# Optimization experiments

Hardware: AMD Instinct MI355X
Metric: run time of the kernel (lower is better)

Reference implementation:

```python
import jax, jax.numpy as jnp
import numpy as np

DIM = 128  # matches init kwarg `dim`; scale = dim ** 0.5


def setup_inputs() -> dict:
    key = jax.random.key(0)
    k1, k2, k3, k4 = jax.random.split(key, 4)
    A = 100000
    K = 1600000  # num edges
    z_msg_all = jax.random.normal(k1, (A, DIM), dtype=jnp.float32)
    recv_query_all = jax.random.normal(k2, (A, DIM), dtype=jnp.float32)
    i_idx = jax.random.randint(k3, (K,), 0, A, dtype=jnp.int64)
    j_idx = jax.random.randint(k4, (K,), 0, A, dtype=jnp.int64)
    return {"z_msg_all": z_msg_all, "recv_query_all": recv_query_all,
            "i_idx": i_idx, "j_idx": j_idx, "A": A}


def reference(z_msg_all, recv_query_all, i_idx, j_idx, A):
    # q_j = z[j], k_i = z[i]; per-edge scores; segmented softmax over recipient j;
    # weighted scatter-add of values k_i into pooled[j]. recv_query_all is unused
    # in the original forward (kept for signature fidelity).
    scale = DIM ** 0.5
    k = z_msg_all[i_idx]                     # (K, D) gather
    q = z_msg_all[j_idx]                     # (K, D) gather
    scores = jnp.sum(q * k, axis=-1) / scale  # (K,)
    # segmented softmax (3-pass: amax, exp, sum)
    max_per = jax.ops.segment_max(scores, j_idx, num_segments=A)  # (A,)
    exp = jnp.exp(scores - max_per[j_idx])                         # (K,)
    denom = jax.ops.segment_sum(exp, j_idx, num_segments=A)        # (A,)
    alpha = exp / (denom[j_idx] + 1e-6)                            # (K,)
    # weighted scatter-add of values into recipients
    pooled = jax.ops.segment_sum(alpha[:, None] * k, j_idx, num_segments=A)  # (A, D)
    return pooled
```

## Files before the change

### kernel.cpp

```cpp
#include <hip/hip_runtime.h>
#include <math.h>


typedef unsigned short us8 __attribute__((ext_vector_type(8)));
typedef float f32x2 __attribute__((ext_vector_type(2)));

#define CAP  8192
#define ABLK 512
#define EPB  (ABLK * 8)

__device__ inline unsigned short f2bf(float f) {
    unsigned u = __float_as_uint(f);
    return (unsigned short)((u + 0x7fff + ((u >> 16) & 1)) >> 16);
}
__device__ inline float bfhi(unsigned u) { return __uint_as_float(u & 0xffff0000u); }
__device__ inline float bflo(unsigned u) { return __uint_as_float(u << 16); }

__global__ __launch_bounds__(ABLK) void bin_kernel(
        const float* __restrict__ z, us8* __restrict__ z16,
        const int* __restrict__ i_idx, const int* __restrict__ j_idx,
        int* __restrict__ gcount, unsigned* __restrict__ binned,
        int n16, int K, int NB) {
    int tid = threadIdx.x;
    int t0 = blockIdx.x * ABLK + tid;
    int nth = gridDim.x * ABLK;

    const float4* __restrict__ z4 = reinterpret_cast<const float4*>(z);
    #pragma unroll
    for (int q = 0; q < 8; ++q) {
        int t = t0 + q * nth;
        if (t < n16) {
            float4 a = z4[(size_t)2 * t];
            float4 c = z4[(size_t)2 * t + 1];
            us8 o;
            o[0] = f2bf(a.x); o[1] = f2bf(a.y); o[2] = f2bf(a.z); o[3] = f2bf(a.w);
            o[4] = f2bf(c.x); o[5] = f2bf(c.y); o[6] = f2bf(c.z); o[7] = f2bf(c.w);
            z16[t] = o;
        }
    }

    __shared__ int lhist[ABLK];
    __shared__ int loff[ABLK + 1];
    __shared__ int lcur[ABLK];
    __shared__ int gbase[ABLK];
    __shared__ unsigned staged_p[EPB];
    __shared__ unsigned short staged_b[EPB];

    lhist[tid] = 0;
    __syncthreads();

    int ebase = blockIdx.x * EPB;
    int myi[8], myj[8], myb[8];
    #pragma unroll
    for (int q = 0; q < 8; ++q) {
        int e = ebase + tid + q * ABLK;
        if (e < K) {
            myj[q] = j_idx[e];
            myi[q] = i_idx[e];
            myb[q] = myj[q] >> 8;
            atomicAdd(&lhist[myb[q]], 1);
        } else {
            myb[q] = -1;
        }
    }
    __syncthreads();
    for (int off = 1; off < ABLK; off <<= 1) {
        int v = (tid >= off) ? lhist[tid - off] : 0;
        __syncthreads();
        lhist[tid] += v;
        __syncthreads();
    }
    loff[tid + 1] = lhist[tid];
    if (tid == 0) loff[0] = 0;
    __syncthreads();
    int cntb = loff[tid + 1] - loff[tid];
    if (tid < NB && cntb > 0)
        gbase[tid] = tid * CAP + atomicAdd(&gcount[tid], cntb);
    lcur[tid] = loff[tid];
    __syncthreads();
    #pragma unroll
    for (int q = 0; q < 8; ++q) {
        if (myb[q] >= 0) {
            int p = atomicAdd(&lcur[myb[q]], 1);
            staged_p[p] = ((unsigned)myi[q] << 8) | ((unsigned)myj[q] & 255u);
            staged_b[p] = (unsigned short)myb[q];
        }
    }
    __syncthreads();
    int totE = loff[ABLK];
    for (int idx = tid; idx < totE; idx += ABLK) {
        int bb = staged_b[idx];
        binned[(size_t)gbase[bb] + (idx - loff[bb])] = staged_p[idx];
    }
}

__global__ __launch_bounds__(1024) void finish_kernel(
        unsigned* __restrict__ binned, const int* __restrict__ gcount,
        int2* __restrict__ seg, int A) {
    __shared__ unsigned staged[CAP];
    __shared__ int sorted_loc[CAP];
    __shared__ int hist[256];
    __shared__ int offs[257];
    __shared__ int cur[256];

    int b = blockIdx.x;
    int tid = threadIdx.x;
    int cnt = gcount[b];
    if (cnt > CAP) cnt = CAP;
    unsigned* __restrict__ src = binned + (size_t)b * CAP;

    if (tid < 256) hist[tid] = 0;
    for (int x = tid; x < cnt; x += 1024) staged[x] = src[x];
    __syncthreads();
    for (int x = tid; x < cnt; x += 1024)
        atomicAdd(&hist[staged[x] & 255u], 1);
    __syncthreads();
    for (int off = 1; off < 256; off <<= 1) {
        int v = 0;
        if (tid < 256 && tid >= off) v = hist[tid - off];
        __syncthreads();
        if (tid < 256 && tid >= off) hist[tid] += v;
        __syncthreads();
    }
    if (tid == 0) offs[0] = 0;
    if (tid < 256) offs[tid + 1] = hist[tid];
    __syncthreads();
    if (tid < 256) cur[tid] = offs[tid];
    __syncthreads();
    for (int x = tid; x < cnt; x += 1024) {
        unsigned pk = staged[x];
        int p = atomicAdd(&cur[pk & 255u], 1);
        sorted_loc[p] = (int)(pk >> 8);
    }
    __syncthreads();
    for (int x = tid; x < cnt; x += 1024) src[x] = (unsigned)sorted_loc[x];
    if (tid < 256) {
        int j = (b << 8) + tid;
        if (j < A)
            seg[j] = make_int2(b * CAP + offs[tid], b * CAP + offs[tid + 1]);
    }
}

__global__ __launch_bounds__(256) void attn_kernel(
        const float* __restrict__ z, const us8* __restrict__ z16,
        const unsigned* __restrict__ sorted_i, const int2* __restrict__ seg,
        float* __restrict__ out, int A) {
    int w = blockIdx.x * 4 + (threadIdx.x >> 6);
    if (w >= A) return;
    int lane = threadIdx.x & 63;
    int g = lane >> 3;
    int r = lane & 7;

    const float4* __restrict__ z4 = reinterpret_cast<const float4*>(z);
    size_t qb = (size_t)w * 32;
    float4 a0 = z4[qb + 2 * r];
    float4 a1 = z4[qb + 2 * r + 1];
    float4 a2 = z4[qb + 16 + 2 * r];
    float4 a3 = z4[qb + 16 + 2 * r + 1];
    const float scale = 0.08838834764831843f;
    f32x2 q2[8];
    q2[0] = f32x2{a0.x, a0.y} * scale;  q2[1] = f32x2{a0.z, a0.w} * scale;
    q2[2] = f32x2{a1.x, a1.y} * scale;  q2[3] = f32x2{a1.z, a1.w} * scale;
    q2[4] = f32x2{a2.x, a2.y} * scale;  q2[5] = f32x2{a2.z, a2.w} * scale;
    q2[6] = f32x2{a3.x, a3.y} * scale;  q2[7] = f32x2{a3.z, a3.w} * scale;

    int2 s01 = seg[w];

    float l = 0.0f;
    f32x2 acc[8];
    #pragma unroll
    for (int t = 0; t < 8; ++t) acc[t] = f32x2{0.f, 0.f};

    const uint4* __restrict__ zk = reinterpret_cast<const uint4*>(z16);
    for (int p = s01.x + g; p < s01.y; p += 8) {
        int i = (int)sorted_i[p];
        uint4 u0 = zk[(size_t)i * 16 + r];
        uint4 u1 = zk[(size_t)i * 16 + 8 + r];
        f32x2 k2[8];
        k2[0] = f32x2{bflo(u0.x), bfhi(u0.x)};
        k2[1] = f32x2{bflo(u0.y), bfhi(u0.y)};
        k2[2] = f32x2{bflo(u0.z), bfhi(u0.z)};
        k2[3] = f32x2{bflo(u0.w), bfhi(u0.w)};
        k2[4] = f32x2{bflo(u1.x), bfhi(u1.x)};
        k2[5] = f32x2{bflo(u1.y), bfhi(u1.y)};
        k2[6] = f32x2{bflo(u1.z), bfhi(u1.z)};
        k2[7] = f32x2{bflo(u1.w), bfhi(u1.w)};

        f32x2 prod = q2[0] * k2[0];
        #pragma unroll
        for (int t = 1; t < 8; ++t) prod += q2[t] * k2[t];
        float part = prod.x + prod.y;
        part += __shfl_xor(part, 1);
        part += __shfl_xor(part, 2);
        part += __shfl_xor(part, 4);

        float pe = __expf(part);
        l += pe;
        f32x2 pe2 = {pe, pe};
        #pragma unroll
        for (int t = 0; t < 8; ++t) acc[t] += pe2 * k2[t];
    }

    l += __shfl_xor(l, 8);
    l += __shfl_xor(l, 16);
    l += __shfl_xor(l, 32);

    {
        bool hi = (g & 4) != 0;
        #pragma unroll
        for (int t = 0; t < 4; ++t) {
            f32x2 send = hi ? acc[t] : acc[t + 4];
            f32x2 recv;
            recv.x = __shfl_xor(send.x, 32);
            recv.y = __shfl_xor(send.y, 32);
            f32x2 keep = hi ? acc[t + 4] : acc[t];
            acc[t] = keep + recv;
        }
        hi = (g & 2) != 0;
        #pragma unroll
        for (int t = 0; t < 2; ++t) {
            f32x2 send = hi ? acc[t] : acc[t + 2];
            f32x2 recv;
            recv.x = __shfl_xor(send.x, 16);
            recv.y = __shfl_xor(send.y, 16);
            f32x2 keep = hi ? acc[t + 2] : acc[t];
            acc[t] = keep + recv;
        }
        hi = (g & 1) != 0;
        {
            f32x2 send = hi ? acc[0] : acc[1];
            f32x2 recv;
            recv.x = __shfl_xor(send.x, 8);
            recv.y = __shfl_xor(send.y, 8);
            f32x2 keep = hi ? acc[1] : acc[0];
            acc[0] = keep + recv;
        }
    }

    float inv = 1.0f / (l + 1e-6f);
    float2 o;
    o.x = acc[0].x * inv;
    o.y = acc[0].y * inv;
    int o_idx = ((g & 4) << 3) + 4 * r + (g & 3);
    reinterpret_cast<float2*>(out)[(size_t)w * 64 + o_idx] = o;
}

extern "C" void kernel_launch(void* const* d_in, const int* in_sizes, int n_in,
                              void* d_out, int out_size, void* d_ws, size_t ws_size,
                              hipStream_t stream) {
    const float* z     = (const float*)d_in[0];
    const int*   i_idx = (const int*)d_in[2];
    const int*   j_idx = (const int*)d_in[3];

    const int D = 128;
    int A = in_sizes[0] / D;
    int K = in_sizes[2];
    int n16 = A * (D / 8);
    int NB = (A + 255) >> 8;

    unsigned short* z16 = (unsigned short*)d_ws;
    unsigned* binned = (unsigned*)(z16 + (size_t)A * 128);
    int2* seg = (int2*)(binned + (size_t)NB * CAP);
    int* gcount = (int*)(seg + A);

    float* out = (float*)d_out;

    hipMemsetAsync(gcount, 0, (size_t)NB * sizeof(int), stream);
    int gA = (K + EPB - 1) / EPB;
    int gC = (n16 + EPB - 1) / EPB;
    if (gC > gA) gA = gC;
    bin_kernel<<<gA, ABLK, 0, stream>>>(z, (us8*)z16, i_idx, j_idx,
                                        gcount, binned, n16, K, NB);
    finish_kernel<<<NB, 1024, 0, stream>>>(binned, gcount, seg, A);
    attn_kernel<<<(A + 3) / 4, 256, 0, stream>>>(z, (const us8*)z16, binned,
                                                 seg, out, A);
}
```

Measured before the change: 114.9 us.

## Move bf16 conversion to finish kernel, halve edges per bin block, prefetch indices

Moves the fp32-to-bf16 conversion of z out of the binning kernel into the per-bin sort kernel, which uses a grid-stride loop. The binning kernel now handles 2048 edges per block instead of 4096, so it launches more blocks with lower per-block latency. The attention kernel now reads the query from the bf16 copy instead of fp32, which drops the fp32 z read but lowers query precision. It also folds log2(e) into the scale so it can use exp2f, and software-prefetches the next sorted index. The prefetch reads up to 8 entries past each segment end; that stays inside the binned buffer but is an unguarded read.

```diff
diff --git a/kernel.cpp b/kernel.cpp
--- a/kernel.cpp
+++ b/kernel.cpp
@@ -5,9 +5,9 @@
 typedef unsigned short us8 __attribute__((ext_vector_type(8)));
 typedef float f32x2 __attribute__((ext_vector_type(2)));
 
-#define CAP  8192
-#define ABLK 512
-#define EPB  (ABLK * 8)
+#define CAP   8192
+#define ABLK  512
+#define EPB   2048
 
 __device__ inline unsigned short f2bf(float f) {
     unsigned u = __float_as_uint(f);
@@ -17,27 +17,10 @@
 __device__ inline float bflo(unsigned u) { return __uint_as_float(u << 16); }
 
 __global__ __launch_bounds__(ABLK) void bin_kernel(
-        const float* __restrict__ z, us8* __restrict__ z16,
         const int* __restrict__ i_idx, const int* __restrict__ j_idx,
         int* __restrict__ gcount, unsigned* __restrict__ binned,
-        int n16, int K, int NB) {
+        int K, int NB) {
     int tid = threadIdx.x;
-    int t0 = blockIdx.x * ABLK + tid;
-    int nth = gridDim.x * ABLK;
-
-    const float4* __restrict__ z4 = reinterpret_cast<const float4*>(z);
-    #pragma unroll
-    for (int q = 0; q < 8; ++q) {
-        int t = t0 + q * nth;
-        if (t < n16) {
-            float4 a = z4[(size_t)2 * t];
-            float4 c = z4[(size_t)2 * t + 1];
-            us8 o;
-            o[0] = f2bf(a.x); o[1] = f2bf(a.y); o[2] = f2bf(a.z); o[3] = f2bf(a.w);
-            o[4] = f2bf(c.x); o[5] = f2bf(c.y); o[6] = f2bf(c.z); o[7] = f2bf(c.w);
-            z16[t] = o;
-        }
-    }
 
     __shared__ int lhist[ABLK];
     __shared__ int loff[ABLK + 1];
@@ -50,9 +33,9 @@
     __syncthreads();
 
     int ebase = blockIdx.x * EPB;
-    int myi[8], myj[8], myb[8];
+    int myi[4], myj[4], myb[4];
     #pragma unroll
-    for (int q = 0; q < 8; ++q) {
+    for (int q = 0; q < 4; ++q) {
         int e = ebase + tid + q * ABLK;
         if (e < K) {
             myj[q] = j_idx[e];
@@ -79,7 +62,7 @@
     lcur[tid] = loff[tid];
     __syncthreads();
     #pragma unroll
-    for (int q = 0; q < 8; ++q) {
+    for (int q = 0; q < 4; ++q) {
         if (myb[q] >= 0) {
             int p = atomicAdd(&lcur[myb[q]], 1);
             staged_p[p] = ((unsigned)myi[q] << 8) | ((unsigned)myj[q] & 255u);
@@ -95,8 +78,9 @@
 }
 
 __global__ __launch_bounds__(1024) void finish_kernel(
+        const float* __restrict__ z, us8* __restrict__ z16,
         unsigned* __restrict__ binned, const int* __restrict__ gcount,
-        int2* __restrict__ seg, int A) {
+        int2* __restrict__ seg, int A, int n16) {
     __shared__ unsigned staged[CAP];
     __shared__ int sorted_loc[CAP];
     __shared__ int hist[256];
@@ -105,6 +89,20 @@
 
     int b = blockIdx.x;
     int tid = threadIdx.x;
+
+    {
+        const float4* __restrict__ z4 = reinterpret_cast<const float4*>(z);
+        int gstride = gridDim.x * 1024;
+        for (int t = b * 1024 + tid; t < n16; t += gstride) {
+            float4 a = z4[(size_t)2 * t];
+            float4 c = z4[(size_t)2 * t + 1];
+            us8 o;
+            o[0] = f2bf(a.x); o[1] = f2bf(a.y); o[2] = f2bf(a.z); o[3] = f2bf(a.w);
+            o[4] = f2bf(c.x); o[5] = f2bf(c.y); o[6] = f2bf(c.z); o[7] = f2bf(c.w);
+            z16[t] = o;
+        }
+    }
+
     int cnt = gcount[b];
     if (cnt > CAP) cnt = CAP;
     unsigned* __restrict__ src = binned + (size_t)b * CAP;
@@ -142,7 +140,7 @@
 }
 
 __global__ __launch_bounds__(256) void attn_kernel(
-        const float* __restrict__ z, const us8* __restrict__ z16,
+        const us8* __restrict__ z16,
         const unsigned* __restrict__ sorted_i, const int2* __restrict__ seg,
         float* __restrict__ out, int A) {
     int w = blockIdx.x * 4 + (threadIdx.x >> 6);
@@ -151,18 +149,20 @@
     int g = lane >> 3;
     int r = lane & 7;
 
-    const float4* __restrict__ z4 = reinterpret_cast<const float4*>(z);
-    size_t qb = (size_t)w * 32;
-    float4 a0 = z4[qb + 2 * r];
-    float4 a1 = z4[qb + 2 * r + 1];
-    float4 a2 = z4[qb + 16 + 2 * r];
-    float4 a3 = z4[qb + 16 + 2 * r + 1];
-    const float scale = 0.08838834764831843f;
+    const uint4* __restrict__ zk = reinterpret_cast<const uint4*>(z16);
+    const float scale = 0.08838834764831843f * 1.4426950408889634f;
+
+    uint4 uq0 = zk[(size_t)w * 16 + r];
+    uint4 uq1 = zk[(size_t)w * 16 + 8 + r];
     f32x2 q2[8];
-    q2[0] = f32x2{a0.x, a0.y} * scale;  q2[1] = f32x2{a0.z, a0.w} * scale;
-    q2[2] = f32x2{a1.x, a1.y} * scale;  q2[3] = f32x2{a1.z, a1.w} * scale;
-    q2[4] = f32x2{a2.x, a2.y} * scale;  q2[5] = f32x2{a2.z, a2.w} * scale;
-    q2[6] = f32x2{a3.x, a3.y} * scale;  q2[7] = f32x2{a3.z, a3.w} * scale;
+    q2[0] = f32x2{bflo(uq0.x), bfhi(uq0.x)} * scale;
+    q2[1] = f32x2{bflo(uq0.y), bfhi(uq0.y)} * scale;
+    q2[2] = f32x2{bflo(uq0.z), bfhi(uq0.z)} * scale;
+    q2[3] = f32x2{bflo(uq0.w), bfhi(uq0.w)} * scale;
+    q2[4] = f32x2{bflo(uq1.x), bfhi(uq1.x)} * scale;
+    q2[5] = f32x2{bflo(uq1.y), bfhi(uq1.y)} * scale;
+    q2[6] = f32x2{bflo(uq1.z), bfhi(uq1.z)} * scale;
+    q2[7] = f32x2{bflo(uq1.w), bfhi(uq1.w)} * scale;
 
     int2 s01 = seg[w];
 
@@ -171,9 +171,11 @@
     #pragma unroll
     for (int t = 0; t < 8; ++t) acc[t] = f32x2{0.f, 0.f};
 
-    const uint4* __restrict__ zk = reinterpret_cast<const uint4*>(z16);
-    for (int p = s01.x + g; p < s01.y; p += 8) {
-        int i = (int)sorted_i[p];
+    int p = s01.x + g;
+    int i_next = (int)sorted_i[p];
+    while (p < s01.y) {
+        int i = i_next;
+        i_next = (int)sorted_i[p + 8];
         uint4 u0 = zk[(size_t)i * 16 + r];
         uint4 u1 = zk[(size_t)i * 16 + 8 + r];
         f32x2 k2[8];
@@ -194,11 +196,12 @@
         part += __shfl_xor(part, 2);
         part += __shfl_xor(part, 4);
 
-        float pe = __expf(part);
+        float pe = exp2f(part);
         l += pe;
         f32x2 pe2 = {pe, pe};
         #pragma unroll
         for (int t = 0; t < 8; ++t) acc[t] += pe2 * k2[t];
+        p += 8;
     }
 
     l += __shfl_xor(l, 8);
@@ -266,12 +269,10 @@
     float* out = (float*)d_out;
 
     hipMemsetAsync(gcount, 0, (size_t)NB * sizeof(int), stream);
-    int gA = (K + EPB - 1) / EPB;
-    int gC = (n16 + EPB - 1) / EPB;
-    if (gC > gA) gA = gC;
-    bin_kernel<<<gA, ABLK, 0, stream>>>(z, (us8*)z16, i_idx, j_idx,
-                                        gcount, binned, n16, K, NB);
-    finish_kernel<<<NB, 1024, 0, stream>>>(binned, gcount, seg, A);
-    attn_kernel<<<(A + 3) / 4, 256, 0, stream>>>(z, (const us8*)z16, binned,
+    bin_kernel<<<(K + EPB - 1) / EPB, ABLK, 0, stream>>>(i_idx, j_idx,
+                                                         gcount, binned, K, NB);
+    finish_kernel<<<NB, 1024, 0, stream>>>(z, (us8*)z16, binned, gcount, seg,
+                                           A, n16);
+    attn_kernel<<<(A + 3) / 4, 256, 0, stream>>>((const us8*)z16, binned,
                                                  seg, out, A);
 }
```

After: 120.3 us. 1.05x slower.
